# Kernel optimization log

Measured on AMD Instinct MI355X. Metric: run time of the kernel, lower is better.

## Reference

```python
import jax, jax.numpy as jnp
import numpy as np

N = 4096      # (num_domains+1) * batch_size
F_IN = 512    # nfeat
HID = 64      # nhid per head
H = 8         # nheads
ALPHA = 0.2   # leaky-relu negative slope
EDGE_P = 0.01 # adjacency density


def setup_inputs() -> dict:
    key = jax.random.key(0)
    k1, k2, k3, k4 = jax.random.split(key, 4)
    x = jax.random.normal(k1, (N, F_IN), dtype=jnp.float32)
    adj = (jax.random.uniform(k2, (N, N)) < EDGE_P).astype(jnp.float32)
    # ensure self-loops so every row has at least one valid edge for softmax
    adj = jnp.maximum(adj, jnp.eye(N, dtype=jnp.float32))
    W = jax.random.normal(k3, (H, F_IN, HID), dtype=jnp.float32) * 0.1
    a = jax.random.normal(k4, (H, 2 * HID), dtype=jnp.float32) * 0.1
    return {"x": x, "adj": adj, "W": W, "a": a}


def reference(x, adj, W, a):
    # Wh: [H, N, HID] -- per-head linear projection
    Wh = jnp.einsum('nf,hfd->hnd', x, W)
    # additive attention logits: e_ij = leakyrelu(a1.Wh_i + a2.Wh_j)
    e_src = jnp.einsum('hnd,hd->hn', Wh, a[:, :HID])   # [H, N]
    e_dst = jnp.einsum('hnd,hd->hn', Wh, a[:, HID:])   # [H, N]
    e = jax.nn.leaky_relu(e_src[:, :, None] + e_dst[:, None, :], ALPHA)  # [H, N, N]
    e = jnp.where(adj[None] > 0, e, jnp.float32(-9e15))
    att = jax.nn.softmax(e, axis=-1)                    # masked softmax over neighbors
    h = jnp.einsum('hnm,hmd->hnd', att, Wh)             # [H, N, HID]
    h = jax.nn.elu(h)                                   # concat=True -> elu per head
    # concat heads: [N, H*HID]
    return jnp.transpose(h, (1, 0, 2)).reshape(N, H * HID)
```

## Files before the change

### kernel.cpp

```cpp
#include <hip/hip_runtime.h>
#include <hip/hip_bf16.h>
#include <math.h>

#define N_NODES 4096
#define F_IN    512
#define HID     64
#define H       8
#define NJ      512
#define ALPHA   0.2f
#define MAXN    128

typedef __bf16 bf16x8 __attribute__((ext_vector_type(8)));
typedef float  f32x4  __attribute__((ext_vector_type(4)));

#define A_CHUNKS (N_NODES * F_IN / 8)
#define B_CHUNKS (NJ * F_IN / 8)
#define PREP_BLOCKS ((A_CHUNKS + B_CHUNKS) / 256)

__global__ __launch_bounds__(256) void prep_compact(const float* __restrict__ x,
                                                    const float* __restrict__ W,
                                                    const float* __restrict__ adj,
                                                    __bf16* __restrict__ AhT,
                                                    __bf16* __restrict__ AlT,
                                                    __bf16* __restrict__ BthT,
                                                    int* __restrict__ nbr_g,
                                                    int* __restrict__ cnt_g) {
    if (blockIdx.x < N_NODES) {
        const int i    = blockIdx.x;
        const int tid  = threadIdx.x;
        const int lane = tid & 63;
        __shared__ int nbr[MAXN];
        __shared__ int cnt;
        if (tid == 0) cnt = 0;
        __syncthreads();

        const unsigned long long lt = (1ull << lane) - 1ull;
        const float4* arow = (const float4*)(adj + (size_t)i * N_NODES);
        float4 q[4];
        #pragma unroll
        for (int cc = 0; cc < 4; cc++) q[cc] = arow[cc * 256 + tid];
        #pragma unroll
        for (int cc = 0; cc < 4; cc++) {
            unsigned long long b0 = __ballot(q[cc].x > 0.f);
            unsigned long long b1 = __ballot(q[cc].y > 0.f);
            unsigned long long b2 = __ballot(q[cc].z > 0.f);
            unsigned long long b3 = __ballot(q[cc].w > 0.f);
            int c0 = __popcll(b0), c1 = __popcll(b1), c2 = __popcll(b2), c3 = __popcll(b3);
            int base = 0;
            if (lane == 0) base = atomicAdd(&cnt, c0 + c1 + c2 + c3);
            base = __shfl(base, 0);
            int col = (cc * 256 + tid) * 4;
            if (q[cc].x > 0.f) nbr[base + __popcll(b0 & lt)] = col;
            base += c0;
            if (q[cc].y > 0.f) nbr[base + __popcll(b1 & lt)] = col + 1;
            base += c1;
            if (q[cc].z > 0.f) nbr[base + __popcll(b2 & lt)] = col + 2;
            base += c2;
            if (q[cc].w > 0.f) nbr[base + __popcll(b3 & lt)] = col + 3;
        }
        __syncthreads();
        const int n = cnt;
        if (tid < n) nbr_g[i * MAXN + tid] = nbr[tid];
        if (tid == 0) cnt_g[i] = n;
        return;
    }

    int id = (blockIdx.x - N_NODES) * 256 + threadIdx.x;
    if (id < A_CHUNKS) {
        int u  = id & 511;
        int kt = (id >> 9) & 7;
        int bm = id >> 12;
        int r  = u >> 3, c8 = u & 7;
        int col = kt * 64 + ((c8 ^ (r & 7)) << 3);
        const float4* gp = (const float4*)(x + (size_t)(bm * 64 + r) * F_IN + col);
        float4 v0 = gp[0];
        float4 v1 = gp[1];
        float vv[8] = {v0.x, v0.y, v0.z, v0.w, v1.x, v1.y, v1.z, v1.w};
        bf16x8 hv, lv;
        #pragma unroll
        for (int e = 0; e < 8; e++) {
            __bf16 hi = (__bf16)vv[e];
            hv[e] = hi;
            lv[e] = (__bf16)(vv[e] - (float)hi);
        }
        *(bf16x8*)(AhT + (size_t)id * 8) = hv;
        *(bf16x8*)(AlT + (size_t)id * 8) = lv;
    } else {
        int bid = id - A_CHUNKS;
        if (bid < B_CHUNKS) {
            int u  = bid & 511;
            int kt = (bid >> 9) & 7;
            int h  = bid >> 12;
            int r  = u >> 3, c8 = u & 7;
            int kb = kt * 64 + ((c8 ^ (r & 7)) << 3);
            bf16x8 hv;
            #pragma unroll
            for (int e = 0; e < 8; e++) {
                hv[e] = (__bf16)W[((size_t)h * F_IN + kb + e) * HID + r];
            }
            *(bf16x8*)(BthT + (size_t)bid * 8) = hv;
        }
    }
}

__device__ __forceinline__ void async16(void* lds, const void* g) {
    __builtin_amdgcn_global_load_lds(
        (const __attribute__((address_space(1))) unsigned int*)g,
        (__attribute__((address_space(3))) unsigned int*)lds, 16, 0, 0);
}

__global__ __launch_bounds__(256) void wh_gemm(const __bf16* __restrict__ AhT,
                                               const __bf16* __restrict__ AlT,
                                               const __bf16* __restrict__ BthT,
                                               const float* __restrict__ a,
                                               __bf16* __restrict__ Whb,
                                               float* __restrict__ esrc,
                                               float* __restrict__ edst) {
    const int bid = blockIdx.x;
    const int xcd = bid & 7;
    const int s0  = bid >> 3;
    const int bm  = xcd * 8 + (s0 >> 3);
    const int h   = s0 & 7;

    const int tid  = threadIdx.x;
    const int wave = tid >> 6;
    const int lane = tid & 63;
    const int lm = lane & 15;
    const int lq = lane >> 4;

    __shared__ __align__(16) __bf16 smem[2 * 3 * 4096];

    f32x4 acc[4];
    #pragma unroll
    for (int c = 0; c < 4; c++) acc[c] = (f32x4){0.f, 0.f, 0.f, 0.f};

    const __bf16* tA_h = AhT  + (size_t)bm * (8 * 4096);
    const __bf16* tA_l = AlT  + (size_t)bm * (8 * 4096);
    const __bf16* tB   = BthT + (size_t)h  * (8 * 4096);

    const int rowA = wave * 16 + lm;

    auto stage = [&](int buf, int kt2) {
        __bf16* base = smem + buf * 12288;
        const size_t ko = (size_t)kt2 * 4096;
        #pragma unroll
        for (int s = 0; s < 2; s++) {
            int u  = s * 256 + tid;
            int ub = s * 256 + wave * 64;
            async16(base +        ub * 8, tA_h + ko + (size_t)u * 8);
            async16(base + 4096 + ub * 8, tA_l + ko + (size_t)u * 8);
            async16(base + 8192 + ub * 8, tB   + ko + (size_t)u * 8);
        }
    };

    stage(0, 0);

    for (int kt = 0; kt < 8; kt++) {
        const int cur = kt & 1;
        if (kt < 7) {
            stage(1 - cur, kt + 1);
            asm volatile("s_waitcnt vmcnt(6)" ::: "memory");
        } else {
            asm volatile("s_waitcnt vmcnt(0)" ::: "memory");
        }
        __builtin_amdgcn_s_barrier();
        __builtin_amdgcn_sched_barrier(0);

        const __bf16* Ash = smem + cur * 12288;
        const __bf16* Asl = Ash + 4096;
        const __bf16* Bsh = Ash + 8192;

        #pragma unroll
        for (int kh = 0; kh < 2; kh++) {
            const int ce = (((kh << 2) + lq) ^ (lm & 7)) << 3;
            bf16x8 afh = *(const bf16x8*)&Ash[rowA * 64 + ce];
            bf16x8 afl = *(const bf16x8*)&Asl[rowA * 64 + ce];
            bf16x8 bh[4];
            #pragma unroll
            for (int c = 0; c < 4; c++) {
                bh[c] = *(const bf16x8*)&Bsh[(c * 16 + lm) * 64 + ce];
            }
            #pragma unroll
            for (int c = 0; c < 4; c++) {
                acc[c] = __builtin_amdgcn_mfma_f32_16x16x32_bf16(afh, bh[c], acc[c], 0, 0, 0);
                acc[c] = __builtin_amdgcn_mfma_f32_16x16x32_bf16(afl, bh[c], acc[c], 0, 0, 0);
            }
        }
        __builtin_amdgcn_s_barrier();
    }

    float a1c[4], a2c[4];
    #pragma unroll
    for (int c = 0; c < 4; c++) {
        a1c[c] = a[h * 2 * HID + c * 16 + lm];
        a2c[c] = a[h * 2 * HID + HID + c * 16 + lm];
    }

    #pragma unroll
    for (int r = 0; r < 4; r++) {
        int row = bm * 64 + wave * 16 + lq * 4 + r;
        float s1 = 0.f, s2 = 0.f;
        #pragma unroll
        for (int c = 0; c < 4; c++) {
            float v = acc[c][r];
            Whb[(size_t)row * NJ + h * HID + c * 16 + lm] = (__bf16)v;
            s1 += v * a1c[c];
            s2 += v * a2c[c];
        }
        #pragma unroll
        for (int o = 1; o < 16; o <<= 1) {
            s1 += __shfl_xor(s1, o);
            s2 += __shfl_xor(s2, o);
        }
        if (lm == 0) {
            esrc[h * N_NODES + row] = s1;
            edst[h * N_NODES + row] = s2;
        }
    }
}

__global__ __launch_bounds__(256) void gat_attn(const int* __restrict__ nbr_g,
                                                const int* __restrict__ cnt_g,
                                                const __bf16* __restrict__ Whb,
                                                const float* __restrict__ esrc,
                                                const float* __restrict__ edst,
                                                float* __restrict__ out) {
    const int i    = blockIdx.x;
    const int tid  = threadIdx.x;
    const int wave = tid >> 6;
    const int lane = tid & 63;
    __shared__ int    nbr[MAXN];
    __shared__ __align__(8)  float2 an[H][MAXN];
    __shared__ float  denom[H];
    __shared__ __align__(16) float4 part[128];

    const int n = cnt_g[i];
    if (tid < n) nbr[tid] = nbr_g[i * MAXN + tid];
    __syncthreads();

    #pragma unroll
    for (int k = 0; k < 2; k++) {
        const int h = wave * 2 + k;
        float es = esrc[h * N_NODES + i];
        float m = -1e30f;
        for (int j = lane; j < n; j += 64) {
            int c = nbr[j];
            float lg = es + edst[h * N_NODES + c];
            lg = lg > 0.f ? lg : ALPHA * lg;
            an[h][j] = make_float2(lg, __int_as_float(c << 10));
            m = fmaxf(m, lg);
        }
        #pragma unroll
        for (int o = 32; o; o >>= 1) m = fmaxf(m, __shfl_xor(m, o));
        float s = 0.f;
        for (int j = lane; j < n; j += 64) {
            float w = __expf(an[h][j].x - m);
            an[h][j].x = w;
            s += w;
        }
        #pragma unroll
        for (int o = 32; o; o >>= 1) s += __shfl_xor(s, o);
        if (lane == 0) denom[h] = s;
    }
    __syncthreads();

    const int qd = tid >> 7;
    const int t  = tid & 127;
    const int h  = t >> 4;
    const char* wp = (const char*)Whb + t * 8;
    float a0 = 0.f, a1 = 0.f, a2 = 0.f, a3 = 0.f;
    #pragma unroll 4
    for (int j = qd; j < n; j += 2) {
        float2 p = an[h][j];
        uint2 u = *(const uint2*)(wp + __float_as_uint(p.y));
        float w = p.x;
        a0 += w * __uint_as_float(u.x << 16);
        a1 += w * __uint_as_float(u.x & 0xffff0000u);
        a2 += w * __uint_as_float(u.y << 16);
        a3 += w * __uint_as_float(u.y & 0xffff0000u);
    }
    if (qd) part[t] = make_float4(a0, a1, a2, a3);
    __syncthreads();
    if (qd == 0) {
        float4 p = part[t];
        a0 += p.x; a1 += p.y; a2 += p.z; a3 += p.w;
        float inv = 1.f / denom[h];
        a0 *= inv; a1 *= inv; a2 *= inv; a3 *= inv;
        a0 = a0 > 0.f ? a0 : expm1f(a0);
        a1 = a1 > 0.f ? a1 : expm1f(a1);
        a2 = a2 > 0.f ? a2 : expm1f(a2);
        a3 = a3 > 0.f ? a3 : expm1f(a3);
        *(float4*)(out + (size_t)i * NJ + t * 4) = make_float4(a0, a1, a2, a3);
    }
}

extern "C" void kernel_launch(void* const* d_in, const int* in_sizes, int n_in,
                              void* d_out, int out_size, void* d_ws, size_t ws_size,
                              hipStream_t stream) {
    const float* x   = (const float*)d_in[0];
    const float* adj = (const float*)d_in[1];
    const float* W   = (const float*)d_in[2];
    const float* a   = (const float*)d_in[3];
    float* out = (float*)d_out;

    float*  esrc = (float*)d_ws;
    float*  edst = esrc + (size_t)H * N_NODES;
    __bf16* Whb  = (__bf16*)(edst + (size_t)H * N_NODES);
    __bf16* AhT  = Whb + (size_t)N_NODES * NJ;
    __bf16* AlT  = AhT + (size_t)N_NODES * F_IN;
    __bf16* BthT = AlT + (size_t)N_NODES * F_IN;
    int*    nbr_g = (int*)(BthT + (size_t)NJ * F_IN);
    int*    cnt_g = nbr_g + (size_t)N_NODES * MAXN;

    prep_compact<<<N_NODES + PREP_BLOCKS, 256, 0, stream>>>(x, W, adj, AhT, AlT, BthT,
                                                            nbr_g, cnt_g);

    wh_gemm<<<512, 256, 0, stream>>>(AhT, AlT, BthT, a, Whb, esrc, edst);

    gat_attn<<<N_NODES, 256, 0, stream>>>(nbr_g, cnt_g, Whb, esrc, edst, out);
}
```

Measured before the change: 131.4 us.

## Move adjacency compaction into GEMM launch and use one wave per row

Adjacency-row compaction leaves the x/W conversion kernel and now runs as extra blocks appended to the Wh GEMM grid. Because it is independent of the GEMM, its adj streaming can overlap the GEMM's compute instead of running before it. Compaction now uses one wave per row with a running ballot prefix and writes straight to global memory, which removes the shared-memory atomics and block barriers. The trade-off is that the conversion kernel gets shorter while the GEMM grid gets longer, and the compaction blocks reserve the GEMM's large shared-memory footprint, which may limit how many run at once.

```diff
diff --git a/kernel.cpp b/kernel.cpp
--- a/kernel.cpp
+++ b/kernel.cpp
@@ -17,55 +17,12 @@
 #define B_CHUNKS (NJ * F_IN / 8)
 #define PREP_BLOCKS ((A_CHUNKS + B_CHUNKS) / 256)
 
-__global__ __launch_bounds__(256) void prep_compact(const float* __restrict__ x,
-                                                    const float* __restrict__ W,
-                                                    const float* __restrict__ adj,
-                                                    __bf16* __restrict__ AhT,
-                                                    __bf16* __restrict__ AlT,
-                                                    __bf16* __restrict__ BthT,
-                                                    int* __restrict__ nbr_g,
-                                                    int* __restrict__ cnt_g) {
-    if (blockIdx.x < N_NODES) {
-        const int i    = blockIdx.x;
-        const int tid  = threadIdx.x;
-        const int lane = tid & 63;
-        __shared__ int nbr[MAXN];
-        __shared__ int cnt;
-        if (tid == 0) cnt = 0;
-        __syncthreads();
-
-        const unsigned long long lt = (1ull << lane) - 1ull;
-        const float4* arow = (const float4*)(adj + (size_t)i * N_NODES);
-        float4 q[4];
-        #pragma unroll
-        for (int cc = 0; cc < 4; cc++) q[cc] = arow[cc * 256 + tid];
-        #pragma unroll
-        for (int cc = 0; cc < 4; cc++) {
-            unsigned long long b0 = __ballot(q[cc].x > 0.f);
-            unsigned long long b1 = __ballot(q[cc].y > 0.f);
-            unsigned long long b2 = __ballot(q[cc].z > 0.f);
-            unsigned long long b3 = __ballot(q[cc].w > 0.f);
-            int c0 = __popcll(b0), c1 = __popcll(b1), c2 = __popcll(b2), c3 = __popcll(b3);
-            int base = 0;
-            if (lane == 0) base = atomicAdd(&cnt, c0 + c1 + c2 + c3);
-            base = __shfl(base, 0);
-            int col = (cc * 256 + tid) * 4;
-            if (q[cc].x > 0.f) nbr[base + __popcll(b0 & lt)] = col;
-            base += c0;
-            if (q[cc].y > 0.f) nbr[base + __popcll(b1 & lt)] = col + 1;
-            base += c1;
-            if (q[cc].z > 0.f) nbr[base + __popcll(b2 & lt)] = col + 2;
-            base += c2;
-            if (q[cc].w > 0.f) nbr[base + __popcll(b3 & lt)] = col + 3;
-        }
-        __syncthreads();
-        const int n = cnt;
-        if (tid < n) nbr_g[i * MAXN + tid] = nbr[tid];
-        if (tid == 0) cnt_g[i] = n;
-        return;
-    }
-
-    int id = (blockIdx.x - N_NODES) * 256 + threadIdx.x;
+__global__ __launch_bounds__(256) void conv_prep(const float* __restrict__ x,
+                                                 const float* __restrict__ W,
+                                                 __bf16* __restrict__ AhT,
+                                                 __bf16* __restrict__ AlT,
+                                                 __bf16* __restrict__ BthT) {
+    int id = blockIdx.x * 256 + threadIdx.x;
     if (id < A_CHUNKS) {
         int u  = id & 511;
         int kt = (id >> 9) & 7;
@@ -109,26 +66,57 @@
         (__attribute__((address_space(3))) unsigned int*)lds, 16, 0, 0);
 }
 
-__global__ __launch_bounds__(256) void wh_gemm(const __bf16* __restrict__ AhT,
-                                               const __bf16* __restrict__ AlT,
-                                               const __bf16* __restrict__ BthT,
-                                               const float* __restrict__ a,
-                                               __bf16* __restrict__ Whb,
-                                               float* __restrict__ esrc,
-                                               float* __restrict__ edst) {
+__global__ __launch_bounds__(256) void gemm_compact(const __bf16* __restrict__ AhT,
+                                                    const __bf16* __restrict__ AlT,
+                                                    const __bf16* __restrict__ BthT,
+                                                    const float* __restrict__ a,
+                                                    const float* __restrict__ adj,
+                                                    __bf16* __restrict__ Whb,
+                                                    float* __restrict__ esrc,
+                                                    float* __restrict__ edst,
+                                                    int* __restrict__ nbr_g,
+                                                    int* __restrict__ cnt_g) {
+    __shared__ __align__(16) __bf16 smem[2 * 3 * 4096];
+
     const int bid = blockIdx.x;
+    const int tid  = threadIdx.x;
+    const int wave = tid >> 6;
+    const int lane = tid & 63;
+
+    if (bid >= 512) {
+        const int i = (bid - 512) * 4 + wave;
+        const unsigned long long lt = (1ull << lane) - 1ull;
+        const float4* arow = (const float4*)(adj + (size_t)i * N_NODES);
+        int* rowp = nbr_g + i * MAXN;
+        int base = 0;
+        #pragma unroll 4
+        for (int cc = 0; cc < 16; cc++) {
+            float4 qv = arow[cc * 64 + lane];
+            unsigned long long b0 = __ballot(qv.x > 0.f);
+            unsigned long long b1 = __ballot(qv.y > 0.f);
+            unsigned long long b2 = __ballot(qv.z > 0.f);
+            unsigned long long b3 = __ballot(qv.w > 0.f);
+            int col = (cc * 64 + lane) * 4;
+            if (qv.x > 0.f) rowp[base + __popcll(b0 & lt)] = col;
+            base += __popcll(b0);
+            if (qv.y > 0.f) rowp[base + __popcll(b1 & lt)] = col + 1;
+            base += __popcll(b1);
+            if (qv.z > 0.f) rowp[base + __popcll(b2 & lt)] = col + 2;
+            base += __popcll(b2);
+            if (qv.w > 0.f) rowp[base + __popcll(b3 & lt)] = col + 3;
+            base += __popcll(b3);
+        }
+        if (lane == 0) cnt_g[i] = base;
+        return;
+    }
+
     const int xcd = bid & 7;
     const int s0  = bid >> 3;
     const int bm  = xcd * 8 + (s0 >> 3);
     const int h   = s0 & 7;
 
-    const int tid  = threadIdx.x;
-    const int wave = tid >> 6;
-    const int lane = tid & 63;
     const int lm = lane & 15;
     const int lq = lane >> 4;
-
-    __shared__ __align__(16) __bf16 smem[2 * 3 * 4096];
 
     f32x4 acc[4];
     #pragma unroll
@@ -312,10 +300,10 @@
     int*    nbr_g = (int*)(BthT + (size_t)NJ * F_IN);
     int*    cnt_g = nbr_g + (size_t)N_NODES * MAXN;
 
-    prep_compact<<<N_NODES + PREP_BLOCKS, 256, 0, stream>>>(x, W, adj, AhT, AlT, BthT,
-                                                            nbr_g, cnt_g);
-
-    wh_gemm<<<512, 256, 0, stream>>>(AhT, AlT, BthT, a, Whb, esrc, edst);
+    conv_prep<<<PREP_BLOCKS, 256, 0, stream>>>(x, W, AhT, AlT, BthT);
+
+    gemm_compact<<<512 + N_NODES / 4, 256, 0, stream>>>(AhT, AlT, BthT, a, adj,
+                                                        Whb, esrc, edst, nbr_g, cnt_g);
 
     gat_attn<<<N_NODES, 256, 0, stream>>>(nbr_g, cnt_g, Whb, esrc, edst, out);
 }
```

Result: slower. 142.1 us (+8.1%).
